# Optimization experiments

Measured on AMD Instinct MI355X. Metric: run time of the kernel, lower is better.

The kernel has to match this reference:

```python
import jax, jax.numpy as jnp
import numpy as np

B, S, D, H, L = 2, 2048, 1024, 16, 4
HD = D // H
EPS = 1e-6
ROPE_BASE = 10000.0


def rms_norm(x, w):
    v = jnp.mean(x.astype(jnp.float32) ** 2, axis=-1, keepdims=True)
    return (w * (x.astype(jnp.float32) * jax.lax.rsqrt(v + EPS))).astype(x.dtype)


def rotate_half(x):
    x1, x2 = jnp.split(x, 2, axis=-1)
    return jnp.concatenate([-x2, x1], axis=-1)


def setup_inputs() -> dict:
    key = jax.random.key(0)
    ks = jax.random.split(key, 8)
    x = jax.random.normal(ks[0], (B, S, D), jnp.float32)
    time_deltas = jax.random.uniform(ks[1], (B, S), jnp.float32)
    # causal multiplicative mask [B, S, S]
    attn_mask = jnp.broadcast_to(jnp.tril(jnp.ones((S, S), jnp.float32)), (B, S, S))
    sd = 0.02
    uvqk_w = jax.random.normal(ks[2], (L, D, 4 * D), jnp.float32) * sd
    uvqk_b = jnp.zeros((L, 4 * D), jnp.float32)
    gate_w = jnp.ones((L, D), jnp.float32)
    out_w = jax.random.normal(ks[3], (L, D, D), jnp.float32) * sd
    out_b = jnp.zeros((L, D), jnp.float32)
    in_norm_w = jnp.ones((D,), jnp.float32)
    last_norm_w = jnp.ones((D,), jnp.float32)
    position_ids = jnp.broadcast_to(jnp.arange(S, dtype=jnp.int32), (B, S))
    return {"x": x, "time_deltas": time_deltas, "attn_mask": attn_mask,
            "uvqk_w": uvqk_w, "uvqk_b": uvqk_b, "gate_w": gate_w,
            "out_w": out_w, "out_b": out_b, "in_norm_w": in_norm_w,
            "last_norm_w": last_norm_w, "position_ids": position_ids}


def reference(x, time_deltas, attn_mask, uvqk_w, uvqk_b, gate_w, out_w, out_b,
              in_norm_w, last_norm_w, position_ids):
    # RotaryEmbedding: combined position = pos + 0.1*log(dt+1)
    inv_freq = 1.0 / ROPE_BASE ** (jnp.arange(0, HD, 2, dtype=jnp.float32) / HD)
    pos = position_ids.astype(jnp.float32) + jnp.log(time_deltas + 1.0) * 0.1
    freqs = pos[..., None] * inv_freq                      # [B,S,HD/2]
    emb = jnp.concatenate([freqs, freqs], axis=-1)          # [B,S,HD]
    cos = jnp.cos(emb)[:, :, None, :]                       # [B,S,1,HD]
    sin = jnp.sin(emb)[:, :, None, :]

    scale = 1.0 / np.sqrt(HD).astype(np.float32)
    h = rms_norm(x, in_norm_w)
    for l in range(L):
        residual = h
        uvqk = h @ uvqk_w[l] + uvqk_b[l]                    # [B,S,4D]
        u, v, q, k = jnp.split(uvqk, 4, axis=-1)
        u = jax.nn.silu(u)
        q = q.reshape(B, S, H, HD)
        k = k.reshape(B, S, H, HD)
        v = v.reshape(B, S, H, HD)
        q = q * cos + rotate_half(q) * sin
        k = k * cos + rotate_half(k) * sin
        scores = jnp.einsum('bqhd,bkhd->bhqk', q, k) * scale
        w = jax.nn.silu(scores) * attn_mask[:, None, :, :]  # SiLU attn, masked
        attn = jnp.einsum('bhqk,bkhd->bqhd', w, v).reshape(B, S, D)
        gated = rms_norm(attn, gate_w[l]) * u
        h = residual + gated @ out_w[l] + out_b[l]
    return rms_norm(h, last_norm_w)
```

## Files before the change

### kernel.cpp

```cpp
#include <hip/hip_runtime.h>
#include <hip/hip_bf16.h>
#include <math.h>

#define BB 2
#define SS 2048
#define DD 1024
#define HH 16
#define HD 64
#define LL 4
#define BS (BB * SS)
#define FOURD (4 * DD)

typedef unsigned int u32;
typedef unsigned short ushort_t;
typedef __attribute__((ext_vector_type(8))) short bf16x8;
typedef __attribute__((ext_vector_type(4))) float f32x4;

__device__ __forceinline__ float silu_f(float x) {
    return x / (1.0f + expf(-x));
}
__device__ __forceinline__ float silu_fast(float x) {
    return x * __builtin_amdgcn_rcpf(1.0f + __expf(-x));
}

__device__ __forceinline__ ushort_t f2bf(float x) {
    u32 u = __float_as_uint(x);
    u32 r = (u + 0x7fffu + ((u >> 16) & 1u)) >> 16;
    return (ushort_t)r;
}
__device__ __forceinline__ float bf2f(ushort_t h) {
    return __uint_as_float((u32)h << 16);
}

typedef __attribute__((address_space(3))) u32 lds_u32;
typedef const __attribute__((address_space(1))) u32 glb_u32;
__device__ __forceinline__ void gload16(const void* g, const void* lds) {
    __builtin_amdgcn_global_load_lds((glb_u32*)(uintptr_t)g,
                                     (lds_u32*)(uintptr_t)lds, 16, 0, 0);
}

#define MFMA16(a, b, c) __builtin_amdgcn_mfma_f32_16x16x32_bf16((a), (b), (c), 0, 0, 0)

union U8 { u32 d[4]; bf16x8 v; };

__global__ __launch_bounds__(256) void rope_table_kernel(
    const float* __restrict__ td, const int* __restrict__ pid,
    float* __restrict__ cosT, float* __restrict__ sinT)
{
    int idx = blockIdx.x * blockDim.x + threadIdx.x;
    if (idx >= BS * 32) return;
    int i = idx & 31, bs = idx >> 5;
    float pos = (float)pid[bs] + 0.1f * logf(td[bs] + 1.0f);
    float inv = powf(10000.0f, -(float)(2 * i) / 64.0f);
    float f = pos * inv;
    float c = cosf(f), s = sinf(f);
    cosT[bs * HD + i] = c;  cosT[bs * HD + i + 32] = c;
    sinT[bs * HD + i] = s;  sinT[bs * HD + i + 32] = s;
}

__global__ __launch_bounds__(256) void rmsnorm_kernel(
    const float* __restrict__ in, const float* __restrict__ w,
    const float* __restrict__ mul, int mulStride,
    float* __restrict__ out,
    ushort_t* __restrict__ hi, ushort_t* __restrict__ lo)
{
    __shared__ float red[4];
    int row = blockIdx.x, t = threadIdx.x;
    const float4 v = *(const float4*)&in[(size_t)row * DD + t * 4];
    float ss = v.x * v.x + v.y * v.y + v.z * v.z + v.w * v.w;
    #pragma unroll
    for (int o = 32; o > 0; o >>= 1) ss += __shfl_down(ss, o);
    if ((t & 63) == 0) red[t >> 6] = ss;
    __syncthreads();
    float tot = red[0] + red[1] + red[2] + red[3];
    float r = rsqrtf(tot * (1.0f / (float)DD) + 1e-6f);
    const float4 wv = *(const float4*)&w[t * 4];
    float4 o4;
    o4.x = v.x * r * wv.x;  o4.y = v.y * r * wv.y;
    o4.z = v.z * r * wv.z;  o4.w = v.w * r * wv.w;
    if (mul) {
        const float4 m = *(const float4*)&mul[(size_t)row * mulStride + t * 4];
        o4.x *= m.x; o4.y *= m.y; o4.z *= m.z; o4.w *= m.w;
    }
    const size_t o = (size_t)row * DD + t * 4;
    *(float4*)&out[o] = o4;
    if (hi) {
        ushort4 h4, l4;
        float e;
        h4.x = f2bf(o4.x); e = o4.x - bf2f(h4.x); l4.x = f2bf(e);
        h4.y = f2bf(o4.y); e = o4.y - bf2f(h4.y); l4.y = f2bf(e);
        h4.z = f2bf(o4.z); e = o4.z - bf2f(h4.z); l4.z = f2bf(e);
        h4.w = f2bf(o4.w); e = o4.w - bf2f(h4.w); l4.w = f2bf(e);
        *(ushort4*)&hi[o] = h4;
        *(ushort4*)&lo[o] = l4;
    }
}

__global__ __launch_bounds__(256) void wsplit_kernel(
    const float* __restrict__ W, ushort_t* __restrict__ hi,
    ushort_t* __restrict__ lo, int K, int N)
{
    __shared__ float T[32][33];
    const int n0 = blockIdx.x * 32, k0 = blockIdx.y * 32;
    const int t = threadIdx.x;
    {
        const int r = t >> 3, cg = (t & 7) * 4;
        const float4 v = *(const float4*)&W[(size_t)(k0 + r) * N + n0 + cg];
        T[r][cg] = v.x; T[r][cg + 1] = v.y; T[r][cg + 2] = v.z; T[r][cg + 3] = v.w;
    }
    __syncthreads();
    {
        const int n = t >> 3, kg = (t & 7) * 4;
        ushort4 h4, l4;
        float x, e;
        x = T[kg + 0][n]; h4.x = f2bf(x); e = x - bf2f(h4.x); l4.x = f2bf(e);
        x = T[kg + 1][n]; h4.y = f2bf(x); e = x - bf2f(h4.y); l4.y = f2bf(e);
        x = T[kg + 2][n]; h4.z = f2bf(x); e = x - bf2f(h4.z); l4.z = f2bf(e);
        x = T[kg + 3][n]; h4.w = f2bf(x); e = x - bf2f(h4.w); l4.w = f2bf(e);
        const size_t o = (size_t)(n0 + n) * K + k0 + kg;
        *(ushort4*)&hi[o] = h4;
        *(ushort4*)&lo[o] = l4;
    }
}

#define TBM 128
#define TBN 128
#define TBK 32
__global__ __launch_bounds__(256) void gemm3_kernel(
    const ushort_t* __restrict__ Ah, const ushort_t* __restrict__ Al,
    const ushort_t* __restrict__ Bh, const ushort_t* __restrict__ Bl,
    const float* __restrict__ bias, const float* __restrict__ res,
    float* __restrict__ C, ushort_t* __restrict__ Chi, ushort_t* __restrict__ Clo,
    int M, int N, int K)
{
    __shared__ ushort_t sAh[TBM][TBK];
    __shared__ ushort_t sAl[TBM][TBK];
    __shared__ ushort_t sBh[TBN][TBK];
    __shared__ ushort_t sBl[TBN][TBK];

    const int tid = threadIdx.x;
    const int w = tid >> 6, l = tid & 63;
    const int wr = w >> 1, wc = w & 1;
    const int m0 = blockIdx.y * TBM, n0 = blockIdx.x * TBN;
    const int lr = l & 15, lk = (l >> 4) * 8;

    f32x4 acc[4][4];
    #pragma unroll
    for (int m = 0; m < 4; ++m)
        #pragma unroll
        for (int n = 0; n < 4; ++n)
            acc[m][n] = (f32x4){0.f, 0.f, 0.f, 0.f};

    for (int k0 = 0; k0 < K; k0 += TBK) {
        if (k0) __syncthreads();
        #pragma unroll
        for (int i = 0; i < 2; ++i) {
            const int cb = i * 256 + w * 64;
            const int chunk = cb + l;
            const int row = chunk >> 2;
            const int kc = (chunk & 3) * 8;
            const size_t ga = (size_t)(m0 + row) * K + k0 + kc;
            const size_t gb = (size_t)(n0 + row) * K + k0 + kc;
            gload16(Ah + ga, &sAh[0][0] + (size_t)cb * 8);
            gload16(Al + ga, &sAl[0][0] + (size_t)cb * 8);
            gload16(Bh + gb, &sBh[0][0] + (size_t)cb * 8);
            gload16(Bl + gb, &sBl[0][0] + (size_t)cb * 8);
        }
        __syncthreads();

        bf16x8 ah[4], al[4], bh[4], bl[4];
        #pragma unroll
        for (int m = 0; m < 4; ++m) {
            ah[m] = *(const bf16x8*)&sAh[wr * 64 + m * 16 + lr][lk];
            al[m] = *(const bf16x8*)&sAl[wr * 64 + m * 16 + lr][lk];
        }
        #pragma unroll
        for (int n = 0; n < 4; ++n) {
            bh[n] = *(const bf16x8*)&sBh[wc * 64 + n * 16 + lr][lk];
            bl[n] = *(const bf16x8*)&sBl[wc * 64 + n * 16 + lr][lk];
        }
        #pragma unroll
        for (int m = 0; m < 4; ++m) {
            #pragma unroll
            for (int n = 0; n < 4; ++n) {
                acc[m][n] = MFMA16(ah[m], bh[n], acc[m][n]);
                acc[m][n] = MFMA16(al[m], bh[n], acc[m][n]);
                acc[m][n] = MFMA16(ah[m], bl[n], acc[m][n]);
            }
        }
    }

    #pragma unroll
    for (int m = 0; m < 4; ++m) {
        #pragma unroll
        for (int n = 0; n < 4; ++n) {
            const int col = n0 + wc * 64 + n * 16 + lr;
            #pragma unroll
            for (int r = 0; r < 4; ++r) {
                const int row = m0 + wr * 64 + m * 16 + (l >> 4) * 4 + r;
                const size_t o = (size_t)row * N + col;
                float v = acc[m][n][r] + bias[col];
                if (res) v += res[o];
                C[o] = v;
                if (Chi) {
                    ushort_t hv = f2bf(v);
                    Chi[o] = hv;
                    Clo[o] = f2bf(v - bf2f(hv));
                }
            }
        }
    }
}

__global__ __launch_bounds__(256) void postproc_kernel(
    float* __restrict__ uvqk,
    const float* __restrict__ cosT, const float* __restrict__ sinT,
    ushort_t* __restrict__ q_hi, ushort_t* __restrict__ q_lo,
    ushort_t* __restrict__ k_hi, ushort_t* __restrict__ k_lo)
{
    const int bs = blockIdx.x, t = threadIdx.x;
    const int b = bs >> 11, s = bs & (SS - 1);
    float* base = uvqk + (size_t)bs * FOURD;

    float4 u = *(float4*)&base[t * 4];
    u.x = silu_f(u.x); u.y = silu_f(u.y); u.z = silu_f(u.z); u.w = silu_f(u.w);
    *(float4*)&base[t * 4] = u;

    const int hh = t >> 4, p = (t & 15) * 2;
    const float c0 = cosT[bs * HD + p], c1 = cosT[bs * HD + p + 1];
    const float s0 = sinT[bs * HD + p], s1 = sinT[bs * HD + p + 1];
    const size_t hrow = ((size_t)(b * HH + hh) * SS + s) * HD;
    #pragma unroll
    for (int sect = 2; sect <= 3; ++sect) {
        const float* qp = base + sect * DD + hh * HD;
        const float a0 = qp[p], a1 = qp[p + 1];
        const float b0 = qp[p + 32], b1 = qp[p + 33];
        float o0 = a0 * c0 - b0 * s0;
        float o1 = a1 * c1 - b1 * s1;
        float o2 = b0 * c0 + a0 * s0;
        float o3 = b1 * c1 + a1 * s1;
        ushort_t* dh = (sect == 2) ? q_hi : k_hi;
        ushort_t* dl = (sect == 2) ? q_lo : k_lo;
        const ushort_t h0 = f2bf(o0), h1 = f2bf(o1);
        const ushort_t h2 = f2bf(o2), h3 = f2bf(o3);
        *(u32*)&dh[hrow + p]      = (u32)h0 | ((u32)h1 << 16);
        *(u32*)&dh[hrow + p + 32] = (u32)h2 | ((u32)h3 << 16);
        *(u32*)&dl[hrow + p]      = (u32)f2bf(o0 - bf2f(h0))
                                  | ((u32)f2bf(o1 - bf2f(h1)) << 16);
        *(u32*)&dl[hrow + p + 32] = (u32)f2bf(o2 - bf2f(h2))
                                  | ((u32)f2bf(o3 - bf2f(h3)) << 16);
    }
}

__global__ __launch_bounds__(256) void vtrans_kernel(
    const float* __restrict__ uvqk,
    ushort_t* __restrict__ vT_hi, ushort_t* __restrict__ vT_lo)
{
    __shared__ float T[64][65];
    const int sb = blockIdx.x, h = blockIdx.y, b = blockIdx.z;
    const int t = threadIdx.x;
    const int s0 = sb * 64;
    #pragma unroll
    for (int it = 0; it < 4; ++it) {
        const int idx = it * 256 + t;
        const int row = idx >> 4, c4 = (idx & 15) * 4;
        const float4 v = *(const float4*)&uvqk[
            (size_t)(b * SS + s0 + row) * FOURD + DD + h * HD + c4];
        T[row][c4] = v.x; T[row][c4 + 1] = v.y;
        T[row][c4 + 2] = v.z; T[row][c4 + 3] = v.w;
    }
    __syncthreads();
    const int d = t >> 2, sc = (t & 3) * 16;
    u32 hw[8], lw[8];
    #pragma unroll
    for (int j = 0; j < 8; ++j) {
        const float x0 = T[sc + 2 * j][d];
        const float x1 = T[sc + 2 * j + 1][d];
        const ushort_t h0 = f2bf(x0), h1 = f2bf(x1);
        hw[j] = (u32)h0 | ((u32)h1 << 16);
        lw[j] = (u32)f2bf(x0 - bf2f(h0)) | ((u32)f2bf(x1 - bf2f(h1)) << 16);
    }
    const size_t o = ((size_t)(b * HH + h) * HD + d) * SS + s0 + sc;
    *(uint4*)&vT_hi[o] = make_uint4(hw[0], hw[1], hw[2], hw[3]);
    *(uint4*)&vT_hi[o + 8] = make_uint4(hw[4], hw[5], hw[6], hw[7]);
    *(uint4*)&vT_lo[o] = make_uint4(lw[0], lw[1], lw[2], lw[3]);
    *(uint4*)&vT_lo[o + 8] = make_uint4(lw[4], lw[5], lw[6], lw[7]);
}

__global__ __launch_bounds__(256) void attn_kernel(
    const ushort_t* __restrict__ q_hi, const ushort_t* __restrict__ q_lo,
    const ushort_t* __restrict__ k_hi, const ushort_t* __restrict__ k_lo,
    const ushort_t* __restrict__ vT_hi, const ushort_t* __restrict__ vT_lo,
    float* __restrict__ attnOut)
{
    __shared__ ushort_t sKh[2][64 * 64];
    __shared__ ushort_t sKl[2][64 * 64];
    __shared__ ushort_t sVh[2][64 * 64];
    __shared__ ushort_t sVl[2][64 * 64];

    const int h = blockIdx.y, b = blockIdx.z;
    const int qt = b ? blockIdx.x : (SS / 128 - 1) - blockIdx.x;
    const int tid = threadIdx.x;
    const int w = tid >> 6, l = tid & 63;
    const int lr = l & 15, g = l >> 4;

    const size_t headQ = ((size_t)(b * HH + h) * SS) * HD;
    const size_t headV = ((size_t)(b * HH + h) * HD) * SS;

    bf16x8 qh[2][2], ql[2][2];
    {
        const int qrow0 = qt * 128 + w * 32;
        #pragma unroll
        for (int qf = 0; qf < 2; ++qf)
            #pragma unroll
            for (int ds_ = 0; ds_ < 2; ++ds_) {
                const size_t off = headQ + (size_t)(qrow0 + qf * 16 + lr) * HD
                                   + ds_ * 32 + g * 8;
                qh[qf][ds_] = *(const bf16x8*)&q_hi[off];
                ql[qf][ds_] = *(const bf16x8*)&q_lo[off];
            }
    }

    f32x4 acc[2][4];
    #pragma unroll
    for (int qf = 0; qf < 2; ++qf)
        #pragma unroll
        for (int df = 0; df < 4; ++df)
            acc[qf][df] = (f32x4){0.f, 0.f, 0.f, 0.f};

    const int nkt = 2 * qt + 2;

#define STAGE_TILE(pb, kt_)                                                    \
    {                                                                          \
        const ushort_t* kbh = k_hi + headQ + (size_t)(kt_) * 64 * HD;          \
        const ushort_t* kbl = k_lo + headQ + (size_t)(kt_) * 64 * HD;          \
        const ushort_t* vbh = vT_hi + headV + (kt_) * 64;                      \
        const ushort_t* vbl = vT_lo + headV + (kt_) * 64;                      \
        _Pragma("unroll")                                                      \
        for (int rep = 0; rep < 2; ++rep) {                                    \
            const int cb = rep * 256 + w * 64;                                 \
            const int chunk = cb + l;                                          \
            const int row = chunk >> 3, dblk = chunk & 7;                      \
            const int sblk = dblk ^ (row & 7);                                 \
            gload16(kbh + (size_t)row * HD + sblk * 8, &sKh[pb][0] + (size_t)cb * 8); \
            gload16(kbl + (size_t)row * HD + sblk * 8, &sKl[pb][0] + (size_t)cb * 8); \
            gload16(vbh + (size_t)row * SS + sblk * 8, &sVh[pb][0] + (size_t)cb * 8); \
            gload16(vbl + (size_t)row * SS + sblk * 8, &sVl[pb][0] + (size_t)cb * 8); \
        }                                                                      \
    }

    STAGE_TILE(0, 0)
    __syncthreads();

    for (int kt = 0; kt < nkt; ++kt) {
        const int pb = kt & 1;
        if (kt + 1 < nkt) STAGE_TILE(pb ^ 1, kt + 1)

        if (kt * 64 <= qt * 128 + w * 32 + 31) {

        f32x4 sc[4][2];
        #pragma unroll
        for (int f = 0; f < 4; ++f)
            #pragma unroll
            for (int qf = 0; qf < 2; ++qf)
                sc[f][qf] = (f32x4){0.f, 0.f, 0.f, 0.f};

        #pragma unroll
        for (int ds_ = 0; ds_ < 2; ++ds_) {
            bf16x8 kh[4], kl[4];
            #pragma unroll
            for (int f = 0; f < 4; ++f) {
                const int addr = (16 * f + lr) * 64 + (((4 * ds_ + g) ^ (lr & 7)) * 8);
                kh[f] = *(const bf16x8*)&sKh[pb][addr];
                kl[f] = *(const bf16x8*)&sKl[pb][addr];
            }
            #pragma unroll
            for (int f = 0; f < 4; ++f)
                #pragma unroll
                for (int qf = 0; qf < 2; ++qf) {
                    sc[f][qf] = MFMA16(kh[f], qh[qf][ds_], sc[f][qf]);
                    sc[f][qf] = MFMA16(kl[f], qh[qf][ds_], sc[f][qf]);
                    sc[f][qf] = MFMA16(kh[f], ql[qf][ds_], sc[f][qf]);
                }
        }

        u32 pkh[4][2][2], pkl[4][2][2];
        #pragma unroll
        for (int f = 0; f < 4; ++f) {
            #pragma unroll
            for (int qf = 0; qf < 2; ++qf) {
                const int qrow = qt * 128 + w * 32 + qf * 16 + lr;
                float pv[4];
                #pragma unroll
                for (int r = 0; r < 4; ++r) {
                    const int key = kt * 64 + 16 * f + 4 * g + r;
                    const float x = sc[f][qf][r] * 0.125f;
                    pv[r] = (key <= qrow) ? silu_fast(x) : 0.0f;
                }
                #pragma unroll
                for (int t2 = 0; t2 < 2; ++t2) {
                    const u32 u0 = __float_as_uint(pv[2 * t2]);
                    const u32 u1 = __float_as_uint(pv[2 * t2 + 1]);
                    const u32 h0 = u0 >> 16, h1 = u1 >> 16;
                    pkh[f][qf][t2] = h0 | (h1 << 16);
                    const float l0 = pv[2 * t2]     - __uint_as_float(h0 << 16);
                    const float l1 = pv[2 * t2 + 1] - __uint_as_float(h1 << 16);
                    pkl[f][qf][t2] = (__float_as_uint(l0) >> 16)
                                   | ((__float_as_uint(l1) >> 16) << 16);
                }
            }
        }

        #pragma unroll
        for (int s2 = 0; s2 < 2; ++s2) {
            U8 ah[2], al[2];
            #pragma unroll
            for (int qf = 0; qf < 2; ++qf) {
                #pragma unroll
                for (int d = 0; d < 4; ++d) {
                    const int srcLane = lr + 16 * (2 * (g & 1) + (d >> 1));
                    const int t2 = d & 1;
                    int x0 = __shfl((int)pkh[2 * s2][qf][t2], srcLane, 64);
                    int x1 = __shfl((int)pkh[2 * s2 + 1][qf][t2], srcLane, 64);
                    ah[qf].d[d] = (g & 2) ? x1 : x0;
                    x0 = __shfl((int)pkl[2 * s2][qf][t2], srcLane, 64);
                    x1 = __shfl((int)pkl[2 * s2 + 1][qf][t2], srcLane, 64);
                    al[qf].d[d] = (g & 2) ? x1 : x0;
                }
            }
            #pragma unroll
            for (int df = 0; df < 4; ++df) {
                const int vaddr = (16 * df + lr) * 64 + (((4 * s2 + g) ^ (lr & 7)) * 8);
                const bf16x8 vh = *(const bf16x8*)&sVh[pb][vaddr];
                const bf16x8 vl = *(const bf16x8*)&sVl[pb][vaddr];
                #pragma unroll
                for (int qf = 0; qf < 2; ++qf) {
                    acc[qf][df] = MFMA16(ah[qf].v, vh, acc[qf][df]);
                    acc[qf][df] = MFMA16(al[qf].v, vh, acc[qf][df]);
                    acc[qf][df] = MFMA16(ah[qf].v, vl, acc[qf][df]);
                }
            }
        }

        }

        __syncthreads();
    }

    #pragma unroll
    for (int qf = 0; qf < 2; ++qf) {
        #pragma unroll
        for (int df = 0; df < 4; ++df) {
            #pragma unroll
            for (int r = 0; r < 4; ++r) {
                const int row = qt * 128 + w * 32 + qf * 16 + 4 * g + r;
                attnOut[(size_t)(b * SS + row) * DD + h * HD + 16 * df + lr]
                    = acc[qf][df][r];
            }
        }
    }
#undef STAGE_TILE
}

extern "C" void kernel_launch(void* const* d_in, const int* in_sizes, int n_in,
                              void* d_out, int out_size, void* d_ws, size_t ws_size,
                              hipStream_t stream) {
    const float* x           = (const float*)d_in[0];
    const float* td          = (const float*)d_in[1];
    const float* uvqk_w      = (const float*)d_in[3];
    const float* uvqk_b      = (const float*)d_in[4];
    const float* gate_w      = (const float*)d_in[5];
    const float* out_w       = (const float*)d_in[6];
    const float* out_b       = (const float*)d_in[7];
    const float* in_norm_w   = (const float*)d_in[8];
    const float* last_norm_w = (const float*)d_in[9];
    const int*   pid         = (const int*)d_in[10];
    float* out = (float*)d_out;
    char*  ws  = (char*)d_ws;

    const size_t QKV = (size_t)BB * HH * SS * HD;

    float* cosT = (float*)ws;                          ws += (size_t)BS * HD * 4;
    float* sinT = (float*)ws;                          ws += (size_t)BS * HD * 4;
    float* h    = (float*)ws;                          ws += (size_t)BS * DD * 4;
    float* uvqk = (float*)ws;                          ws += (size_t)BS * FOURD * 4;
    float* attn = (float*)ws;                          ws += (size_t)BS * DD * 4;
    ushort_t* h_hi  = (ushort_t*)ws;                   ws += (size_t)BS * DD * 2;
    ushort_t* h_lo  = (ushort_t*)ws;                   ws += (size_t)BS * DD * 2;
    ushort_t* g_hi  = (ushort_t*)ws;                   ws += (size_t)BS * DD * 2;
    ushort_t* g_lo  = (ushort_t*)ws;                   ws += (size_t)BS * DD * 2;
    ushort_t* uWt_hi = (ushort_t*)ws;                  ws += (size_t)FOURD * DD * 2;
    ushort_t* uWt_lo = (ushort_t*)ws;                  ws += (size_t)FOURD * DD * 2;
    ushort_t* oWt_hi = (ushort_t*)ws;                  ws += (size_t)DD * DD * 2;
    ushort_t* oWt_lo = (ushort_t*)ws;                  ws += (size_t)DD * DD * 2;
    ushort_t* q_hi  = (ushort_t*)ws;                   ws += QKV * 2;
    ushort_t* q_lo  = (ushort_t*)ws;                   ws += QKV * 2;
    ushort_t* k_hi  = (ushort_t*)ws;                   ws += QKV * 2;
    ushort_t* k_lo  = (ushort_t*)ws;                   ws += QKV * 2;
    ushort_t* vT_hi = (ushort_t*)ws;                   ws += QKV * 2;
    ushort_t* vT_lo = (ushort_t*)ws;                   ws += QKV * 2;
    (void)ws_size;

    rope_table_kernel<<<(BS * 32 + 255) / 256, 256, 0, stream>>>(td, pid, cosT, sinT);
    rmsnorm_kernel<<<BS, 256, 0, stream>>>(x, in_norm_w, nullptr, 0, h, h_hi, h_lo);

    for (int l = 0; l < LL; ++l) {
        wsplit_kernel<<<dim3(FOURD / 32, DD / 32), 256, 0, stream>>>(
            uvqk_w + (size_t)l * DD * FOURD, uWt_hi, uWt_lo, DD, FOURD);
        gemm3_kernel<<<dim3(FOURD / TBN, BS / TBM), 256, 0, stream>>>(
            h_hi, h_lo, uWt_hi, uWt_lo, uvqk_b + (size_t)l * FOURD,
            nullptr, uvqk, nullptr, nullptr, BS, FOURD, DD);
        postproc_kernel<<<BS, 256, 0, stream>>>(
            uvqk, cosT, sinT, q_hi, q_lo, k_hi, k_lo);
        vtrans_kernel<<<dim3(SS / 64, HH, BB), 256, 0, stream>>>(
            uvqk, vT_hi, vT_lo);
        attn_kernel<<<dim3(SS / 128, HH, BB), 256, 0, stream>>>(
            q_hi, q_lo, k_hi, k_lo, vT_hi, vT_lo, attn);
        rmsnorm_kernel<<<BS, 256, 0, stream>>>(
            attn, gate_w + (size_t)l * DD, uvqk, FOURD, attn, g_hi, g_lo);
        wsplit_kernel<<<dim3(DD / 32, DD / 32), 256, 0, stream>>>(
            out_w + (size_t)l * DD * DD, oWt_hi, oWt_lo, DD, DD);
        gemm3_kernel<<<dim3(DD / TBN, BS / TBM), 256, 0, stream>>>(
            g_hi, g_lo, oWt_hi, oWt_lo, out_b + (size_t)l * DD,
            h, h, h_hi, h_lo, BS, DD, DD);
    }

    rmsnorm_kernel<<<BS, 256, 0, stream>>>(h, last_norm_w, nullptr, 0, out, nullptr, nullptr);
}
```

Baseline: 1.490 ms.

## Fuse RoPE and V-transpose kernels, move SiLU to gate norm, shrink attention key tiles

The separate postproc and V-transpose kernels are merged into one qkv_kernel that applies RoPE to q and k with vectorized loads and transposes V in the same launch. The SiLU on u moves into the gate RMSNorm, which removes an in-place read-modify-write of u. The attention kernel drops its key/value tile from 64 to 32 rows, which halves shared memory, allows finer causal skipping and sets MFMA wave priority with s_setprio. The trade-off is twice as many tile iterations and barriers per attention block.

```diff
diff --git a/kernel.cpp b/kernel.cpp
--- a/kernel.cpp
+++ b/kernel.cpp
@@ -60,7 +60,7 @@
 
 __global__ __launch_bounds__(256) void rmsnorm_kernel(
     const float* __restrict__ in, const float* __restrict__ w,
-    const float* __restrict__ mul, int mulStride,
+    const float* __restrict__ mul, int mulStride, int siluMul,
     float* __restrict__ out,
     ushort_t* __restrict__ hi, ushort_t* __restrict__ lo)
 {
@@ -79,7 +79,11 @@
     o4.x = v.x * r * wv.x;  o4.y = v.y * r * wv.y;
     o4.z = v.z * r * wv.z;  o4.w = v.w * r * wv.w;
     if (mul) {
-        const float4 m = *(const float4*)&mul[(size_t)row * mulStride + t * 4];
+        float4 m = *(const float4*)&mul[(size_t)row * mulStride + t * 4];
+        if (siluMul) {
+            m.x = silu_f(m.x); m.y = silu_f(m.y);
+            m.z = silu_f(m.z); m.w = silu_f(m.w);
+        }
         o4.x *= m.x; o4.y *= m.y; o4.z *= m.z; o4.w *= m.w;
     }
     const size_t o = (size_t)row * DD + t * 4;
@@ -212,54 +216,62 @@
     }
 }
 
-__global__ __launch_bounds__(256) void postproc_kernel(
-    float* __restrict__ uvqk,
+__global__ __launch_bounds__(256) void qkv_kernel(
+    const float* __restrict__ uvqk,
     const float* __restrict__ cosT, const float* __restrict__ sinT,
     ushort_t* __restrict__ q_hi, ushort_t* __restrict__ q_lo,
-    ushort_t* __restrict__ k_hi, ushort_t* __restrict__ k_lo)
-{
-    const int bs = blockIdx.x, t = threadIdx.x;
-    const int b = bs >> 11, s = bs & (SS - 1);
-    float* base = uvqk + (size_t)bs * FOURD;
-
-    float4 u = *(float4*)&base[t * 4];
-    u.x = silu_f(u.x); u.y = silu_f(u.y); u.z = silu_f(u.z); u.w = silu_f(u.w);
-    *(float4*)&base[t * 4] = u;
-
-    const int hh = t >> 4, p = (t & 15) * 2;
-    const float c0 = cosT[bs * HD + p], c1 = cosT[bs * HD + p + 1];
-    const float s0 = sinT[bs * HD + p], s1 = sinT[bs * HD + p + 1];
-    const size_t hrow = ((size_t)(b * HH + hh) * SS + s) * HD;
-    #pragma unroll
-    for (int sect = 2; sect <= 3; ++sect) {
-        const float* qp = base + sect * DD + hh * HD;
-        const float a0 = qp[p], a1 = qp[p + 1];
-        const float b0 = qp[p + 32], b1 = qp[p + 33];
-        float o0 = a0 * c0 - b0 * s0;
-        float o1 = a1 * c1 - b1 * s1;
-        float o2 = b0 * c0 + a0 * s0;
-        float o3 = b1 * c1 + a1 * s1;
-        ushort_t* dh = (sect == 2) ? q_hi : k_hi;
-        ushort_t* dl = (sect == 2) ? q_lo : k_lo;
-        const ushort_t h0 = f2bf(o0), h1 = f2bf(o1);
-        const ushort_t h2 = f2bf(o2), h3 = f2bf(o3);
-        *(u32*)&dh[hrow + p]      = (u32)h0 | ((u32)h1 << 16);
-        *(u32*)&dh[hrow + p + 32] = (u32)h2 | ((u32)h3 << 16);
-        *(u32*)&dl[hrow + p]      = (u32)f2bf(o0 - bf2f(h0))
-                                  | ((u32)f2bf(o1 - bf2f(h1)) << 16);
-        *(u32*)&dl[hrow + p + 32] = (u32)f2bf(o2 - bf2f(h2))
-                                  | ((u32)f2bf(o3 - bf2f(h3)) << 16);
-    }
-}
-
-__global__ __launch_bounds__(256) void vtrans_kernel(
-    const float* __restrict__ uvqk,
+    ushort_t* __restrict__ k_hi, ushort_t* __restrict__ k_lo,
     ushort_t* __restrict__ vT_hi, ushort_t* __restrict__ vT_lo)
 {
     __shared__ float T[64][65];
     const int sb = blockIdx.x, h = blockIdx.y, b = blockIdx.z;
     const int t = threadIdx.x;
     const int s0 = sb * 64;
+
+    {
+        const int tok = t >> 2, d0 = (t & 3) * 8;
+        const int bs = b * SS + s0 + tok;
+        const size_t rowBase = (size_t)bs * FOURD;
+        const size_t hrow = ((size_t)(b * HH + h) * SS + (s0 + tok)) * HD;
+        float c[8], s[8];
+        #pragma unroll
+        for (int j = 0; j < 8; ++j) {
+            c[j] = cosT[(size_t)bs * HD + d0 + j];
+            s[j] = sinT[(size_t)bs * HD + d0 + j];
+        }
+        #pragma unroll
+        for (int sect = 2; sect <= 3; ++sect) {
+            const float* qp = uvqk + rowBase + sect * DD + h * HD;
+            float a[8], bq[8];
+            *(float4*)&a[0]  = *(const float4*)&qp[d0];
+            *(float4*)&a[4]  = *(const float4*)&qp[d0 + 4];
+            *(float4*)&bq[0] = *(const float4*)&qp[d0 + 32];
+            *(float4*)&bq[4] = *(const float4*)&qp[d0 + 36];
+            u32 hwL[4], lwL[4], hwH[4], lwH[4];
+            #pragma unroll
+            for (int j = 0; j < 4; ++j) {
+                float oL0 = a[2*j] * c[2*j] - bq[2*j] * s[2*j];
+                float oL1 = a[2*j+1] * c[2*j+1] - bq[2*j+1] * s[2*j+1];
+                float oH0 = bq[2*j] * c[2*j] + a[2*j] * s[2*j];
+                float oH1 = bq[2*j+1] * c[2*j+1] + a[2*j+1] * s[2*j+1];
+                ushort_t x0 = f2bf(oL0), x1 = f2bf(oL1);
+                hwL[j] = (u32)x0 | ((u32)x1 << 16);
+                lwL[j] = (u32)f2bf(oL0 - bf2f(x0))
+                       | ((u32)f2bf(oL1 - bf2f(x1)) << 16);
+                x0 = f2bf(oH0); x1 = f2bf(oH1);
+                hwH[j] = (u32)x0 | ((u32)x1 << 16);
+                lwH[j] = (u32)f2bf(oH0 - bf2f(x0))
+                       | ((u32)f2bf(oH1 - bf2f(x1)) << 16);
+            }
+            ushort_t* dh = (sect == 2) ? q_hi : k_hi;
+            ushort_t* dl = (sect == 2) ? q_lo : k_lo;
+            *(uint4*)&dh[hrow + d0]      = make_uint4(hwL[0], hwL[1], hwL[2], hwL[3]);
+            *(uint4*)&dh[hrow + d0 + 32] = make_uint4(hwH[0], hwH[1], hwH[2], hwH[3]);
+            *(uint4*)&dl[hrow + d0]      = make_uint4(lwL[0], lwL[1], lwL[2], lwL[3]);
+            *(uint4*)&dl[hrow + d0 + 32] = make_uint4(lwH[0], lwH[1], lwH[2], lwH[3]);
+        }
+    }
+
     #pragma unroll
     for (int it = 0; it < 4; ++it) {
         const int idx = it * 256 + t;
@@ -270,21 +282,23 @@
         T[row][c4 + 2] = v.z; T[row][c4 + 3] = v.w;
     }
     __syncthreads();
-    const int d = t >> 2, sc = (t & 3) * 16;
-    u32 hw[8], lw[8];
-    #pragma unroll
-    for (int j = 0; j < 8; ++j) {
-        const float x0 = T[sc + 2 * j][d];
-        const float x1 = T[sc + 2 * j + 1][d];
-        const ushort_t h0 = f2bf(x0), h1 = f2bf(x1);
-        hw[j] = (u32)h0 | ((u32)h1 << 16);
-        lw[j] = (u32)f2bf(x0 - bf2f(h0)) | ((u32)f2bf(x1 - bf2f(h1)) << 16);
-    }
-    const size_t o = ((size_t)(b * HH + h) * HD + d) * SS + s0 + sc;
-    *(uint4*)&vT_hi[o] = make_uint4(hw[0], hw[1], hw[2], hw[3]);
-    *(uint4*)&vT_hi[o + 8] = make_uint4(hw[4], hw[5], hw[6], hw[7]);
-    *(uint4*)&vT_lo[o] = make_uint4(lw[0], lw[1], lw[2], lw[3]);
-    *(uint4*)&vT_lo[o + 8] = make_uint4(lw[4], lw[5], lw[6], lw[7]);
+    {
+        const int d = t >> 2, sc = (t & 3) * 16;
+        u32 hw[8], lw[8];
+        #pragma unroll
+        for (int j = 0; j < 8; ++j) {
+            const float x0 = T[sc + 2 * j][d];
+            const float x1 = T[sc + 2 * j + 1][d];
+            const ushort_t h0 = f2bf(x0), h1 = f2bf(x1);
+            hw[j] = (u32)h0 | ((u32)h1 << 16);
+            lw[j] = (u32)f2bf(x0 - bf2f(h0)) | ((u32)f2bf(x1 - bf2f(h1)) << 16);
+        }
+        const size_t o = ((size_t)(b * HH + h) * HD + d) * SS + s0 + sc;
+        *(uint4*)&vT_hi[o] = make_uint4(hw[0], hw[1], hw[2], hw[3]);
+        *(uint4*)&vT_hi[o + 8] = make_uint4(hw[4], hw[5], hw[6], hw[7]);
+        *(uint4*)&vT_lo[o] = make_uint4(lw[0], lw[1], lw[2], lw[3]);
+        *(uint4*)&vT_lo[o + 8] = make_uint4(lw[4], lw[5], lw[6], lw[7]);
+    }
 }
 
 __global__ __launch_bounds__(256) void attn_kernel(
@@ -293,10 +307,10 @@
     const ushort_t* __restrict__ vT_hi, const ushort_t* __restrict__ vT_lo,
     float* __restrict__ attnOut)
 {
-    __shared__ ushort_t sKh[2][64 * 64];
-    __shared__ ushort_t sKl[2][64 * 64];
-    __shared__ ushort_t sVh[2][64 * 64];
-    __shared__ ushort_t sVl[2][64 * 64];
+    __shared__ ushort_t sKh[2][32 * 64];
+    __shared__ ushort_t sKl[2][32 * 64];
+    __shared__ ushort_t sVh[2][64 * 32];
+    __shared__ ushort_t sVl[2][64 * 32];
 
     const int h = blockIdx.y, b = blockIdx.z;
     const int qt = b ? blockIdx.x : (SS / 128 - 1) - blockIdx.x;
@@ -328,25 +342,23 @@
         for (int df = 0; df < 4; ++df)
             acc[qf][df] = (f32x4){0.f, 0.f, 0.f, 0.f};
 
-    const int nkt = 2 * qt + 2;
+    const int nkt = 4 * qt + 4;
+
+    const int krow = tid >> 3, kblk = tid & 7;
+    const int ksb  = kblk ^ (krow & 7);
+    const int vrow = tid >> 2, vblk = tid & 3;
+    const int vsb  = vblk ^ (vrow & 3);
 
 #define STAGE_TILE(pb, kt_)                                                    \
     {                                                                          \
-        const ushort_t* kbh = k_hi + headQ + (size_t)(kt_) * 64 * HD;          \
-        const ushort_t* kbl = k_lo + headQ + (size_t)(kt_) * 64 * HD;          \
-        const ushort_t* vbh = vT_hi + headV + (kt_) * 64;                      \
-        const ushort_t* vbl = vT_lo + headV + (kt_) * 64;                      \
-        _Pragma("unroll")                                                      \
-        for (int rep = 0; rep < 2; ++rep) {                                    \
-            const int cb = rep * 256 + w * 64;                                 \
-            const int chunk = cb + l;                                          \
-            const int row = chunk >> 3, dblk = chunk & 7;                      \
-            const int sblk = dblk ^ (row & 7);                                 \
-            gload16(kbh + (size_t)row * HD + sblk * 8, &sKh[pb][0] + (size_t)cb * 8); \
-            gload16(kbl + (size_t)row * HD + sblk * 8, &sKl[pb][0] + (size_t)cb * 8); \
-            gload16(vbh + (size_t)row * SS + sblk * 8, &sVh[pb][0] + (size_t)cb * 8); \
-            gload16(vbl + (size_t)row * SS + sblk * 8, &sVl[pb][0] + (size_t)cb * 8); \
-        }                                                                      \
+        const ushort_t* kbh = k_hi + headQ + (size_t)(kt_) * 32 * HD;          \
+        const ushort_t* kbl = k_lo + headQ + (size_t)(kt_) * 32 * HD;          \
+        const ushort_t* vbh = vT_hi + headV + (kt_) * 32;                      \
+        const ushort_t* vbl = vT_lo + headV + (kt_) * 32;                      \
+        gload16(kbh + (size_t)krow * HD + ksb * 8, &sKh[pb][0] + (size_t)tid * 8); \
+        gload16(kbl + (size_t)krow * HD + ksb * 8, &sKl[pb][0] + (size_t)tid * 8); \
+        gload16(vbh + (size_t)vrow * SS + vsb * 8, &sVh[pb][0] + (size_t)tid * 8); \
+        gload16(vbl + (size_t)vrow * SS + vsb * 8, &sVl[pb][0] + (size_t)tid * 8); \
     }
 
     STAGE_TILE(0, 0)
@@ -356,44 +368,46 @@
         const int pb = kt & 1;
         if (kt + 1 < nkt) STAGE_TILE(pb ^ 1, kt + 1)
 
-        if (kt * 64 <= qt * 128 + w * 32 + 31) {
-
-        f32x4 sc[4][2];
-        #pragma unroll
-        for (int f = 0; f < 4; ++f)
+        if (kt * 32 <= qt * 128 + w * 32 + 31) {
+
+        f32x4 sc[2][2];
+        #pragma unroll
+        for (int f = 0; f < 2; ++f)
             #pragma unroll
             for (int qf = 0; qf < 2; ++qf)
                 sc[f][qf] = (f32x4){0.f, 0.f, 0.f, 0.f};
 
         #pragma unroll
         for (int ds_ = 0; ds_ < 2; ++ds_) {
-            bf16x8 kh[4], kl[4];
-            #pragma unroll
-            for (int f = 0; f < 4; ++f) {
+            bf16x8 kh[2], kl[2];
+            #pragma unroll
+            for (int f = 0; f < 2; ++f) {
                 const int addr = (16 * f + lr) * 64 + (((4 * ds_ + g) ^ (lr & 7)) * 8);
                 kh[f] = *(const bf16x8*)&sKh[pb][addr];
                 kl[f] = *(const bf16x8*)&sKl[pb][addr];
             }
-            #pragma unroll
-            for (int f = 0; f < 4; ++f)
+            __builtin_amdgcn_s_setprio(1);
+            #pragma unroll
+            for (int f = 0; f < 2; ++f)
                 #pragma unroll
                 for (int qf = 0; qf < 2; ++qf) {
                     sc[f][qf] = MFMA16(kh[f], qh[qf][ds_], sc[f][qf]);
                     sc[f][qf] = MFMA16(kl[f], qh[qf][ds_], sc[f][qf]);
                     sc[f][qf] = MFMA16(kh[f], ql[qf][ds_], sc[f][qf]);
                 }
-        }
-
-        u32 pkh[4][2][2], pkl[4][2][2];
-        #pragma unroll
-        for (int f = 0; f < 4; ++f) {
+            __builtin_amdgcn_s_setprio(0);
+        }
+
+        u32 pkh[2][2][2], pkl[2][2][2];
+        #pragma unroll
+        for (int f = 0; f < 2; ++f) {
             #pragma unroll
             for (int qf = 0; qf < 2; ++qf) {
                 const int qrow = qt * 128 + w * 32 + qf * 16 + lr;
                 float pv[4];
                 #pragma unroll
                 for (int r = 0; r < 4; ++r) {
-                    const int key = kt * 64 + 16 * f + 4 * g + r;
+                    const int key = kt * 32 + 16 * f + 4 * g + r;
                     const float x = sc[f][qf][r] * 0.125f;
                     pv[r] = (key <= qrow) ? silu_fast(x) : 0.0f;
                 }
@@ -411,8 +425,7 @@
             }
         }
 
-        #pragma unroll
-        for (int s2 = 0; s2 < 2; ++s2) {
+        {
             U8 ah[2], al[2];
             #pragma unroll
             for (int qf = 0; qf < 2; ++qf) {
@@ -420,25 +433,27 @@
                 for (int d = 0; d < 4; ++d) {
                     const int srcLane = lr + 16 * (2 * (g & 1) + (d >> 1));
                     const int t2 = d & 1;
-                    int x0 = __shfl((int)pkh[2 * s2][qf][t2], srcLane, 64);
-                    int x1 = __shfl((int)pkh[2 * s2 + 1][qf][t2], srcLane, 64);
+                    int x0 = __shfl((int)pkh[0][qf][t2], srcLane, 64);
+                    int x1 = __shfl((int)pkh[1][qf][t2], srcLane, 64);
                     ah[qf].d[d] = (g & 2) ? x1 : x0;
-                    x0 = __shfl((int)pkl[2 * s2][qf][t2], srcLane, 64);
-                    x1 = __shfl((int)pkl[2 * s2 + 1][qf][t2], srcLane, 64);
+                    x0 = __shfl((int)pkl[0][qf][t2], srcLane, 64);
+                    x1 = __shfl((int)pkl[1][qf][t2], srcLane, 64);
                     al[qf].d[d] = (g & 2) ? x1 : x0;
                 }
             }
             #pragma unroll
             for (int df = 0; df < 4; ++df) {
-                const int vaddr = (16 * df + lr) * 64 + (((4 * s2 + g) ^ (lr & 7)) * 8);
+                const int vaddr = (16 * df + lr) * 32 + ((g ^ (lr & 3)) * 8);
                 const bf16x8 vh = *(const bf16x8*)&sVh[pb][vaddr];
                 const bf16x8 vl = *(const bf16x8*)&sVl[pb][vaddr];
+                __builtin_amdgcn_s_setprio(1);
                 #pragma unroll
                 for (int qf = 0; qf < 2; ++qf) {
                     acc[qf][df] = MFMA16(ah[qf].v, vh, acc[qf][df]);
                     acc[qf][df] = MFMA16(al[qf].v, vh, acc[qf][df]);
                     acc[qf][df] = MFMA16(ah[qf].v, vl, acc[qf][df]);
                 }
+                __builtin_amdgcn_s_setprio(0);
             }
         }
 
@@ -502,7 +517,7 @@
     (void)ws_size;
 
     rope_table_kernel<<<(BS * 32 + 255) / 256, 256, 0, stream>>>(td, pid, cosT, sinT);
-    rmsnorm_kernel<<<BS, 256, 0, stream>>>(x, in_norm_w, nullptr, 0, h, h_hi, h_lo);
+    rmsnorm_kernel<<<BS, 256, 0, stream>>>(x, in_norm_w, nullptr, 0, 0, h, h_hi, h_lo);
 
     for (int l = 0; l < LL; ++l) {
         wsplit_kernel<<<dim3(FOURD / 32, DD / 32), 256, 0, stream>>>(
@@ -510,14 +525,12 @@
         gemm3_kernel<<<dim3(FOURD / TBN, BS / TBM), 256, 0, stream>>>(
             h_hi, h_lo, uWt_hi, uWt_lo, uvqk_b + (size_t)l * FOURD,
             nullptr, uvqk, nullptr, nullptr, BS, FOURD, DD);
-        postproc_kernel<<<BS, 256, 0, stream>>>(
-            uvqk, cosT, sinT, q_hi, q_lo, k_hi, k_lo);
-        vtrans_kernel<<<dim3(SS / 64, HH, BB), 256, 0, stream>>>(
-            uvqk, vT_hi, vT_lo);
+        qkv_kernel<<<dim3(SS / 64, HH, BB), 256, 0, stream>>>(
+            uvqk, cosT, sinT, q_hi, q_lo, k_hi, k_lo, vT_hi, vT_lo);
         attn_kernel<<<dim3(SS / 128, HH, BB), 256, 0, stream>>>(
             q_hi, q_lo, k_hi, k_lo, vT_hi, vT_lo, attn);
         rmsnorm_kernel<<<BS, 256, 0, stream>>>(
-            attn, gate_w + (size_t)l * DD, uvqk, FOURD, attn, g_hi, g_lo);
+            attn, gate_w + (size_t)l * DD, uvqk, FOURD, 1, attn, g_hi, g_lo);
         wsplit_kernel<<<dim3(DD / 32, DD / 32), 256, 0, stream>>>(
             out_w + (size_t)l * DD * DD, oWt_hi, oWt_lo, DD, DD);
         gemm3_kernel<<<dim3(DD / TBN, BS / TBM), 256, 0, stream>>>(
@@ -525,5 +538,5 @@
             h, h, h_hi, h_lo, BS, DD, DD);
     }
 
-    rmsnorm_kernel<<<BS, 256, 0, stream>>>(h, last_norm_w, nullptr, 0, out, nullptr, nullptr);
-}
+    rmsnorm_kernel<<<BS, 256, 0, stream>>>(h, last_norm_w, nullptr, 0, 0, out, nullptr, nullptr);
+}
```

After: 1.470 ms. Within noise of the previous version (-1.4%).
